# Performance work log

Hardware: AMD Instinct MI355X
Metric: run time of the kernel (lower is better)

The kernel has to match this reference:

```python
import jax, jax.numpy as jnp
import numpy as np

N, B, D, Q = 32, 36, 2048, 1024  # batch, objects, v_dim, q_dim


def setup_inputs() -> dict:
    key = jax.random.key(0)
    ks = jax.random.split(key, 6)
    sc = 0.02  # small init so ReLU chains stay well-scaled
    return {
        "v": jax.random.normal(ks[0], (N, B, D), jnp.float32),
        "q": jax.random.normal(ks[1], (N, Q), jnp.float32),
        "W1": jax.random.normal(ks[2], (D, D), jnp.float32) * sc,
        "b1": jnp.zeros((D,), jnp.float32),
        "W2": jax.random.normal(ks[3], (D, D), jnp.float32) * sc,
        "b2": jnp.zeros((D,), jnp.float32),
        "W3": jax.random.normal(ks[4], (Q, D), jnp.float32) * sc,
        "b3": jnp.zeros((D,), jnp.float32),
    }


def reference(v, q, W1, b1, W2, b2, W3, b3):
    # FCNet = ReLU(Linear(.)) with weight-norm folded, dropout=0 (eval).
    # Original calls linear3 twice (linear4 unused bug), so q_emb == q_emb2.
    qe = jax.nn.relu(q @ W3 + b3)  # (N, D)
    # pairs[n,i,j] = v[n,i]*qe[n] + v[n,j]*qe[n]  -> (N, B, B, D)
    pairs = (v[:, :, None, :] + v[:, None, :, :]) * qe[:, None, None, :]
    h = jax.nn.relu(jnp.einsum('nijd,de->nije', pairs, W1) + b1)  # linear1
    x = jnp.sum(h, axis=2)  # sum over j relations -> (N, B, D)
    return jax.nn.relu(x @ W2 + b2)  # linear2
```

## Files before the change

kernel.cpp:

```cpp
#include <hip/hip_runtime.h>
#include <stdint.h>

#define N_BATCH 32
#define B_OBJ   36
#define D_DIM   2048
#define Q_DIM   1024

typedef __bf16 bf16x8 __attribute__((ext_vector_type(8)));
typedef float  f32x4  __attribute__((ext_vector_type(4)));

__device__ __forceinline__ uint16_t f2bf(float f) {
    uint32_t u = __builtin_bit_cast(uint32_t, f);
    uint32_t r = (u + 0x7FFFu + ((u >> 16) & 1u)) >> 16;
    return (uint16_t)r;
}

__device__ __forceinline__ void gld_lds16(const void* g, void* l) {
    __builtin_amdgcn_global_load_lds(
        (const __attribute__((address_space(1))) uint32_t*)g,
        (__attribute__((address_space(3))) uint32_t*)l, 16, 0, 0);
}

__global__ __launch_bounds__(256) void transpose_all(
    const float* __restrict__ W1, const float* __restrict__ W2,
    const float* __restrict__ W3,
    uint16_t* __restrict__ W1t, uint16_t* __restrict__ W2t,
    uint16_t* __restrict__ W3t) {
    __shared__ float tile[64][65];
    int gy = blockIdx.y;
    const float* W; uint16_t* Wt; int K, k0;
    if (gy < 32)      { W = W1; Wt = W1t; K = 2048; k0 = gy * 64; }
    else if (gy < 64) { W = W2; Wt = W2t; K = 2048; k0 = (gy - 32) * 64; }
    else              { W = W3; Wt = W3t; K = 1024; k0 = (gy - 64) * 64; }
    int n0 = blockIdx.x * 64;
    int t = threadIdx.x;
    {
        int r = t >> 4, c = (t & 15) * 4;
#pragma unroll
        for (int p = 0; p < 4; ++p)
            *(float4*)&tile[r + p * 16][c] =
                *(const float4*)&W[(size_t)(k0 + r + p * 16) * 2048 + n0 + c];
    }
    __syncthreads();
    {
        int n = t >> 2, kb = (t & 3) * 16;
#pragma unroll
        for (int g4 = 0; g4 < 4; ++g4) {
            int k = kb + g4 * 4;
            ushort4 o;
            o.x = f2bf(tile[k][n]);     o.y = f2bf(tile[k + 1][n]);
            o.z = f2bf(tile[k + 2][n]); o.w = f2bf(tile[k + 3][n]);
            *(ushort4*)&Wt[(size_t)(n0 + n) * K + k0 + k] = o;
        }
    }
}

__global__ __launch_bounds__(256) void qk_gemm(
    const float* __restrict__ q,
    const uint16_t* __restrict__ W3t,
    float* __restrict__ qpart) {
    __shared__ __align__(16) uint16_t As[32][32];
    __shared__ __align__(16) uint16_t Bs[128][32];
    int t = threadIdx.x, lane = t & 63, wave = t >> 6;
    int l15 = lane & 15, quad = lane >> 4;
    int n0 = blockIdx.x * 128;
    int kbase = blockIdx.y * 256;
    f32x4 acc[2][2] = {};
    int ar = t >> 3, ac = (t & 7) * 4;
    int br = t >> 2, bk = (t & 3) * 8;

    for (int k0 = 0; k0 < 256; k0 += 32) {
        __syncthreads();
        float4 av = *(const float4*)&q[(size_t)ar * Q_DIM + kbase + k0 + ac];
        ushort4 a4;
        a4.x = f2bf(av.x); a4.y = f2bf(av.y); a4.z = f2bf(av.z); a4.w = f2bf(av.w);
        *(ushort4*)&As[ar][ac] = a4;
        *(uint4*)&Bs[br][bk]      = *(const uint4*)&W3t[(size_t)(n0 + br) * Q_DIM + kbase + k0 + bk];
        *(uint4*)&Bs[br + 64][bk] = *(const uint4*)&W3t[(size_t)(n0 + br + 64) * Q_DIM + kbase + k0 + bk];
        __syncthreads();
        bf16x8 af[2], bfr[2];
        af[0]  = *(const bf16x8*)&As[l15][quad * 8];
        af[1]  = *(const bf16x8*)&As[16 + l15][quad * 8];
        bfr[0] = *(const bf16x8*)&Bs[wave * 32 + l15][quad * 8];
        bfr[1] = *(const bf16x8*)&Bs[wave * 32 + 16 + l15][quad * 8];
#pragma unroll
        for (int i = 0; i < 2; ++i)
#pragma unroll
            for (int j = 0; j < 2; ++j)
                acc[i][j] = __builtin_amdgcn_mfma_f32_16x16x32_bf16(af[i], bfr[j], acc[i][j], 0, 0, 0);
    }
    float* dst = qpart + (size_t)blockIdx.y * 32 * D_DIM;
#pragma unroll
    for (int i = 0; i < 2; ++i)
#pragma unroll
        for (int j = 0; j < 2; ++j) {
            int n = n0 + wave * 32 + j * 16 + l15;
#pragma unroll
            for (int r = 0; r < 4; ++r)
                dst[(size_t)(i * 16 + quad * 4 + r) * D_DIM + n] = acc[i][j][r];
        }
}

__global__ __launch_bounds__(128) void qe_make_u(
    const float* __restrict__ qpart, const float* __restrict__ b3,
    const float* __restrict__ v, uint16_t* __restrict__ u) {
    int nb = blockIdx.y;
    int d4 = blockIdx.x * 128 + threadIdx.x;
    const float4* p = (const float4*)qpart;
    size_t base = (size_t)nb * 512 + d4;
    float4 s0 = p[base], s1 = p[16384 + base], s2 = p[32768 + base], s3 = p[49152 + base];
    float4 b = ((const float4*)b3)[d4];
    float4 qe;
    qe.x = fmaxf(s0.x + s1.x + s2.x + s3.x + b.x, 0.f);
    qe.y = fmaxf(s0.y + s1.y + s2.y + s3.y + b.y, 0.f);
    qe.z = fmaxf(s0.z + s1.z + s2.z + s3.z + b.z, 0.f);
    qe.w = fmaxf(s0.w + s1.w + s2.w + s3.w + b.w, 0.f);
    const float4* v4 = (const float4*)v;
    ushort4* u4 = (ushort4*)u;
    size_t rb = (size_t)nb * B_OBJ * 512 + d4;
#pragma unroll 4
    for (int i = 0; i < B_OBJ; ++i) {
        float4 vv = v4[rb + (size_t)i * 512];
        ushort4 o;
        o.x = f2bf(vv.x * qe.x);
        o.y = f2bf(vv.y * qe.y);
        o.z = f2bf(vv.z * qe.z);
        o.w = f2bf(vv.w * qe.w);
        u4[rb + (size_t)i * 512] = o;
    }
}

__global__ __launch_bounds__(512) void gemm_batch(
    const uint16_t* __restrict__ A,
    const uint16_t* __restrict__ Bt,
    const float* __restrict__ bias,
    void* __restrict__ Cv,
    int mode) {
    extern __shared__ __align__(16) uint16_t smem[];
    float* yt = (float*)smem;

    int t = threadIdx.x, lane = t & 63, wave = t >> 6;
    int l15 = lane & 15, quad = lane >> 4;
    int wr = wave >> 2, wc = wave & 3;
    int nbp = blockIdx.y;
    int n0 = blockIdx.x * 128;
    const uint16_t* Ab = A + (size_t)nbp * 72 * D_DIM;

    const uint16_t* gp[7];
    int loff[7];
    int wslot = (lane & 3) ^ ((lane >> 2) & 3);
#pragma unroll
    for (int c = 0; c < 7; ++c) {
        int r = wave + 8 * c;
        if (r < 24) {
            int g = r >> 2, h = r & 3;
            int arow = g * 16 + (lane >> 2) - (g >= 3 ? 12 : 0);
            gp[c] = Ab + (size_t)arow * D_DIM + h * 32 + wslot * 8;
            loff[c] = h * 3072 + g * 512;
        } else {
            int rb = r - 24, g = rb >> 2, h = rb & 3;
            int brow = g * 16 + (lane >> 2);
            gp[c] = Bt + (size_t)(n0 + brow) * D_DIM + h * 32 + wslot * 8;
            loff[c] = 12288 + h * 4096 + g * 512;
        }
    }

    f32x4 acc[3][2] = {};
    int rslot = quad ^ (l15 & 3);

#define STAGE(kk, bi)                                            \
    {                                                            \
        _Pragma("unroll")                                        \
        for (int c = 0; c < 7; ++c)                              \
            gld_lds16(gp[c] + (kk), smem + (bi) * 28672 + loff[c]); \
    }

    STAGE(0, 0);
    STAGE(128, 1);
    asm volatile("s_waitcnt vmcnt(7)" ::: "memory");
    __builtin_amdgcn_s_barrier();

    for (int k = 0; k < 16; ++k) {
        int cur = k & 1;
        const uint16_t* As = smem + cur * 28672;
        const uint16_t* Bs = As + 12288;
#pragma unroll
        for (int s = 0; s < 4; ++s) {
            bf16x8 af[3], bfr[2];
#pragma unroll
            for (int i = 0; i < 3; ++i)
                af[i] = *(const bf16x8*)(As + s * 3072 + (wr * 48 + i * 16 + l15) * 32 + rslot * 8);
#pragma unroll
            for (int j = 0; j < 2; ++j)
                bfr[j] = *(const bf16x8*)(Bs + s * 4096 + (wc * 32 + j * 16 + l15) * 32 + rslot * 8);
#pragma unroll
            for (int i = 0; i < 3; ++i)
#pragma unroll
                for (int j = 0; j < 2; ++j)
                    acc[i][j] = __builtin_amdgcn_mfma_f32_16x16x32_bf16(af[i], bfr[j], acc[i][j], 0, 0, 0);
        }
        if (k == 15) break;
        __builtin_amdgcn_s_barrier();
        if (k < 14) {
            STAGE((k + 2) * 128, cur);
            asm volatile("s_waitcnt vmcnt(7)" ::: "memory");
        } else {
            asm volatile("s_waitcnt vmcnt(0)" ::: "memory");
        }
        __builtin_amdgcn_s_barrier();
    }
#undef STAGE

    if (mode == 0) {
        uint16_t* X = (uint16_t*)Cv;
        __syncthreads();
#pragma unroll
        for (int i = 0; i < 3; ++i)
#pragma unroll
            for (int j = 0; j < 2; ++j)
#pragma unroll
                for (int r = 0; r < 4; ++r)
                    yt[(wr * 48 + i * 16 + quad * 4 + r) * 132 + wc * 32 + j * 16 + l15] = acc[i][j][r];
        __syncthreads();
        int col = t & 127, sub = t >> 7;
        int b = sub >> 1, half = sub & 1;
        float bv = bias[n0 + col];
        float z[36];
#pragma unroll
        for (int j = 0; j < 36; ++j) z[j] = yt[(b * 48 + j) * 132 + col];
#pragma unroll
        for (int ii = 0; ii < 18; ++ii) {
            int i = half * 18 + ii;
            float zi = z[i] + bv;
            float s = 0.f;
#pragma unroll
            for (int j = 0; j < 36; ++j) s += fmaxf(zi + z[j], 0.f);
            X[(size_t)((nbp * 2 + b) * B_OBJ + i) * D_DIM + n0 + col] = f2bf(s);
        }
    } else {
        float* O = (float*)Cv;
#pragma unroll
        for (int i = 0; i < 3; ++i)
#pragma unroll
            for (int r = 0; r < 4; ++r) {
                int obj = i * 16 + quad * 4 + r;
                if (obj < B_OBJ) {
#pragma unroll
                    for (int j = 0; j < 2; ++j) {
                        int cc = n0 + wc * 32 + j * 16 + l15;
                        O[(size_t)((nbp * 2 + wr) * B_OBJ + obj) * D_DIM + cc] =
                            fmaxf(acc[i][j][r] + bias[cc], 0.f);
                    }
                }
            }
    }
}

extern "C" void kernel_launch(void* const* d_in, const int* in_sizes, int n_in,
                              void* d_out, int out_size, void* d_ws, size_t ws_size,
                              hipStream_t stream) {
    const float* v  = (const float*)d_in[0];
    const float* q  = (const float*)d_in[1];
    const float* W1 = (const float*)d_in[2];
    const float* b1 = (const float*)d_in[3];
    const float* W2 = (const float*)d_in[4];
    const float* b2 = (const float*)d_in[5];
    const float* W3 = (const float*)d_in[6];
    const float* b3 = (const float*)d_in[7];
    float* out = (float*)d_out;

    char* ws = (char*)d_ws;
    uint16_t* W1t   = (uint16_t*)(ws + 0);
    uint16_t* W2t   = (uint16_t*)(ws + 8388608);
    uint16_t* W3t   = (uint16_t*)(ws + 16777216);
    uint16_t* u     = (uint16_t*)(ws + 16777216);
    float*    qpart = (float*)   (ws + 21495808);
    uint16_t* x     = (uint16_t*)(ws + 22806528);

    static bool attr_done = false;
    if (!attr_done) {
        (void)hipFuncSetAttribute((const void*)gemm_batch,
                                  hipFuncAttributeMaxDynamicSharedMemorySize, 114688);
        attr_done = true;
    }

    transpose_all<<<dim3(32, 80), 256, 0, stream>>>(W1, W2, W3, W1t, W2t, W3t);

    qk_gemm<<<dim3(16, 4), 256, 0, stream>>>(q, W3t, qpart);

    qe_make_u<<<dim3(4, N_BATCH), 128, 0, stream>>>(qpart, b3, v, u);

    gemm_batch<<<dim3(16, 16), 512, 114688, stream>>>(u, W1t, b1, x, 0);

    gemm_batch<<<dim3(16, 16), 512, 114688, stream>>>(x, W2t, b2, out, 1);
}
```

Measured before the change: 168.3 us.

## Triple-buffer gemm_batch LDS pipeline and drop redundant A-row duplication

Switches the batched GEMM from double to triple buffering in LDS, issuing the next stage's global-to-LDS loads before the MFMA compute and removing one barrier per iteration. The A tile is restaged as 72 unique rows with a 128-wide XOR-swizzled layout instead of 96 rows with duplicated overlap, cutting the A loads per stage from 24 to 18 wave-rows. Per-wave vmcnt waits are adjusted for the uneven load counts. LDS use rises to 150KB, which keeps occupancy at one block per CU but removes a sync point and some redundant traffic.

```diff
diff --git a/kernel.cpp b/kernel.cpp
--- a/kernel.cpp
+++ b/kernel.cpp
@@ -152,47 +152,60 @@
 #pragma unroll
     for (int c = 0; c < 7; ++c) {
         int r = wave + 8 * c;
-        if (r < 24) {
-            int g = r >> 2, h = r & 3;
-            int arow = g * 16 + (lane >> 2) - (g >= 3 ? 12 : 0);
-            gp[c] = Ab + (size_t)arow * D_DIM + h * 32 + wslot * 8;
-            loff[c] = h * 3072 + g * 512;
+        int rr = (r < 50) ? r : 0;
+        if (rr < 18) {
+            int row = rr * 4 + (lane >> 4);
+            gp[c] = Ab + (size_t)row * D_DIM + ((lane & 15) ^ (row & 7)) * 8;
+            loff[c] = rr * 512;
         } else {
-            int rb = r - 24, g = rb >> 2, h = rb & 3;
+            int rb = rr - 18, h = rb >> 3, g = rb & 7;
             int brow = g * 16 + (lane >> 2);
             gp[c] = Bt + (size_t)(n0 + brow) * D_DIM + h * 32 + wslot * 8;
-            loff[c] = 12288 + h * 4096 + g * 512;
+            loff[c] = 9216 + h * 4096 + g * 512;
         }
     }
 
     f32x4 acc[3][2] = {};
+    int axor  = (4 * wr + l15) & 7;
     int rslot = quad ^ (l15 & 3);
 
 #define STAGE(kk, bi)                                            \
     {                                                            \
         _Pragma("unroll")                                        \
         for (int c = 0; c < 7; ++c)                              \
-            gld_lds16(gp[c] + (kk), smem + (bi) * 28672 + loff[c]); \
+            if (wave + 8 * c < 50)                               \
+                gld_lds16(gp[c] + (kk), smem + (bi) * 25600 + loff[c]); \
+    }
+#define WAIT_L()                                                      \
+    {                                                                 \
+        if (wave < 2) asm volatile("s_waitcnt vmcnt(7)" ::: "memory");\
+        else          asm volatile("s_waitcnt vmcnt(6)" ::: "memory");\
     }
 
     STAGE(0, 0);
     STAGE(128, 1);
-    asm volatile("s_waitcnt vmcnt(7)" ::: "memory");
+    WAIT_L();
     __builtin_amdgcn_s_barrier();
 
+    int cur = 0;
     for (int k = 0; k < 16; ++k) {
-        int cur = k & 1;
-        const uint16_t* As = smem + cur * 28672;
-        const uint16_t* Bs = As + 12288;
+        if (k < 14) {
+            int stb = (cur >= 1) ? cur - 1 : 2;
+            STAGE((k + 2) * 128, stb);
+        }
+        const uint16_t* As = smem + cur * 25600;
+        const uint16_t* Bs = As + 9216;
 #pragma unroll
         for (int s = 0; s < 4; ++s) {
             bf16x8 af[3], bfr[2];
 #pragma unroll
             for (int i = 0; i < 3; ++i)
-                af[i] = *(const bf16x8*)(As + s * 3072 + (wr * 48 + i * 16 + l15) * 32 + rslot * 8);
+                af[i] = *(const bf16x8*)(As + (wr * 36 + i * 16 + l15) * 128 +
+                                         ((4 * s + quad) ^ axor) * 8);
 #pragma unroll
             for (int j = 0; j < 2; ++j)
-                bfr[j] = *(const bf16x8*)(Bs + s * 4096 + (wc * 32 + j * 16 + l15) * 32 + rslot * 8);
+                bfr[j] = *(const bf16x8*)(Bs + s * 4096 +
+                                          (wc * 32 + j * 16 + l15) * 32 + rslot * 8);
 #pragma unroll
             for (int i = 0; i < 3; ++i)
 #pragma unroll
@@ -200,16 +213,16 @@
                     acc[i][j] = __builtin_amdgcn_mfma_f32_16x16x32_bf16(af[i], bfr[j], acc[i][j], 0, 0, 0);
         }
         if (k == 15) break;
-        __builtin_amdgcn_s_barrier();
         if (k < 14) {
-            STAGE((k + 2) * 128, cur);
-            asm volatile("s_waitcnt vmcnt(7)" ::: "memory");
+            WAIT_L();
         } else {
             asm volatile("s_waitcnt vmcnt(0)" ::: "memory");
         }
         __builtin_amdgcn_s_barrier();
+        cur = (cur < 2) ? cur + 1 : 0;
     }
 #undef STAGE
+#undef WAIT_L
 
     if (mode == 0) {
         uint16_t* X = (uint16_t*)Cv;
@@ -280,7 +293,7 @@
     static bool attr_done = false;
     if (!attr_done) {
         (void)hipFuncSetAttribute((const void*)gemm_batch,
-                                  hipFuncAttributeMaxDynamicSharedMemorySize, 114688);
+                                  hipFuncAttributeMaxDynamicSharedMemorySize, 153600);
         attr_done = true;
     }
 
@@ -290,7 +303,7 @@
 
     qe_make_u<<<dim3(4, N_BATCH), 128, 0, stream>>>(qpart, b3, v, u);
 
-    gemm_batch<<<dim3(16, 16), 512, 114688, stream>>>(u, W1t, b1, x, 0);
-
-    gemm_batch<<<dim3(16, 16), 512, 114688, stream>>>(x, W2t, b2, out, 1);
-}
+    gemm_batch<<<dim3(16, 16), 512, 153600, stream>>>(u, W1t, b1, x, 0);
+
+    gemm_batch<<<dim3(16, 16), 512, 153600, stream>>>(x, W2t, b2, out, 1);
+}
```

Measured after the change: 170.1 us. No clear change (+1.1%).

## Load GEMM B operand directly into registers and shrink LDS staging

Applied to the files above, without the earlier changes.

The batched GEMM now loads the weight (B) fragments straight from global memory into registers each k-step instead of staging them through LDS. Only the A tile goes through LDS, double-buffered with a new XOR swizzle, which cuts dynamic shared memory from 112KB to 52KB. The launch bounds now request more resident blocks. The aim is higher occupancy and less LDS traffic. In exchange, B global loads are no longer shared across waves, which raises redundant global/L2 reads and exposes their latency inside each iteration.

```diff
diff --git a/kernel.cpp b/kernel.cpp
--- a/kernel.cpp
+++ b/kernel.cpp
@@ -130,7 +130,7 @@
     }
 }
 
-__global__ __launch_bounds__(512) void gemm_batch(
+__global__ __launch_bounds__(512, 4) void gemm_batch(
     const uint16_t* __restrict__ A,
     const uint16_t* __restrict__ Bt,
     const float* __restrict__ bias,
@@ -146,70 +146,76 @@
     int n0 = blockIdx.x * 128;
     const uint16_t* Ab = A + (size_t)nbp * 72 * D_DIM;
 
-    const uint16_t* gp[7];
-    int loff[7];
-    int wslot = (lane & 3) ^ ((lane >> 2) & 3);
-#pragma unroll
-    for (int c = 0; c < 7; ++c) {
+    const uint16_t* gpa[3];
+    int ra[3];
+#pragma unroll
+    for (int c = 0; c < 3; ++c) {
         int r = wave + 8 * c;
-        if (r < 24) {
-            int g = r >> 2, h = r & 3;
-            int arow = g * 16 + (lane >> 2) - (g >= 3 ? 12 : 0);
-            gp[c] = Ab + (size_t)arow * D_DIM + h * 32 + wslot * 8;
-            loff[c] = h * 3072 + g * 512;
-        } else {
-            int rb = r - 24, g = rb >> 2, h = rb & 3;
-            int brow = g * 16 + (lane >> 2);
-            gp[c] = Bt + (size_t)(n0 + brow) * D_DIM + h * 32 + wslot * 8;
-            loff[c] = 12288 + h * 4096 + g * 512;
-        }
-    }
+        int rr = (r < 18) ? r : 0;
+        int row = rr * 4 + (lane >> 4);
+        gpa[c] = Ab + (size_t)row * D_DIM + ((lane & 15) ^ (row & 7)) * 8;
+        ra[c] = r;
+    }
+    int L = (wave < 2) ? 3 : 2;
+
+    const uint16_t* bp[2];
+#pragma unroll
+    for (int j = 0; j < 2; ++j)
+        bp[j] = Bt + (size_t)(n0 + wc * 32 + j * 16 + l15) * D_DIM + quad * 8;
 
     f32x4 acc[3][2] = {};
-    int rslot = quad ^ (l15 & 3);
-
-#define STAGE(kk, bi)                                            \
-    {                                                            \
-        _Pragma("unroll")                                        \
-        for (int c = 0; c < 7; ++c)                              \
-            gld_lds16(gp[c] + (kk), smem + (bi) * 28672 + loff[c]); \
-    }
-
-    STAGE(0, 0);
-    STAGE(128, 1);
-    asm volatile("s_waitcnt vmcnt(7)" ::: "memory");
-    __builtin_amdgcn_s_barrier();
+    int axor = (4 * wr + l15) & 7;
+
+#define STAGE_A(kk, bi)                                              \
+    {                                                                \
+        _Pragma("unroll")                                            \
+        for (int c = 0; c < 3; ++c)                                  \
+            if (ra[c] < 18)                                          \
+                gld_lds16(gpa[c] + (kk), smem + (bi) * 9216 + ra[c] * 512); \
+    }
+#define WAIT_L()                                                      \
+    {                                                                 \
+        if (wave < 2) asm volatile("s_waitcnt vmcnt(3)" ::: "memory");\
+        else          asm volatile("s_waitcnt vmcnt(2)" ::: "memory");\
+    }
+
+    STAGE_A(0, 0);
 
     for (int k = 0; k < 16; ++k) {
         int cur = k & 1;
-        const uint16_t* As = smem + cur * 28672;
-        const uint16_t* Bs = As + 12288;
-#pragma unroll
-        for (int s = 0; s < 4; ++s) {
-            bf16x8 af[3], bfr[2];
-#pragma unroll
-            for (int i = 0; i < 3; ++i)
-                af[i] = *(const bf16x8*)(As + s * 3072 + (wr * 48 + i * 16 + l15) * 32 + rslot * 8);
-#pragma unroll
-            for (int j = 0; j < 2; ++j)
-                bfr[j] = *(const bf16x8*)(Bs + s * 4096 + (wc * 32 + j * 16 + l15) * 32 + rslot * 8);
-#pragma unroll
-            for (int i = 0; i < 3; ++i)
-#pragma unroll
-                for (int j = 0; j < 2; ++j)
-                    acc[i][j] = __builtin_amdgcn_mfma_f32_16x16x32_bf16(af[i], bfr[j], acc[i][j], 0, 0, 0);
-        }
-        if (k == 15) break;
-        __builtin_amdgcn_s_barrier();
-        if (k < 14) {
-            STAGE((k + 2) * 128, cur);
-            asm volatile("s_waitcnt vmcnt(7)" ::: "memory");
+        int k0 = k * 128;
+        uint4 breg[2][4];
+#pragma unroll
+        for (int j = 0; j < 2; ++j)
+#pragma unroll
+            for (int s = 0; s < 4; ++s)
+                breg[j][s] = *(const uint4*)(bp[j] + k0 + s * 32);
+        if (k < 15) {
+            STAGE_A((k + 1) * 128, cur ^ 1);
+            WAIT_L();
         } else {
             asm volatile("s_waitcnt vmcnt(0)" ::: "memory");
         }
         __builtin_amdgcn_s_barrier();
-    }
-#undef STAGE
+        const uint16_t* Asb = smem + cur * 9216;
+#pragma unroll
+        for (int s = 0; s < 4; ++s) {
+            bf16x8 af[3];
+#pragma unroll
+            for (int i = 0; i < 3; ++i)
+                af[i] = *(const bf16x8*)(Asb + (wr * 36 + i * 16 + l15) * 128 +
+                                         ((4 * s + quad) ^ axor) * 8);
+#pragma unroll
+            for (int i = 0; i < 3; ++i)
+#pragma unroll
+                for (int j = 0; j < 2; ++j)
+                    acc[i][j] = __builtin_amdgcn_mfma_f32_16x16x32_bf16(
+                        af[i], __builtin_bit_cast(bf16x8, breg[j][s]), acc[i][j], 0, 0, 0);
+        }
+        if (k < 15) __builtin_amdgcn_s_barrier();
+    }
+#undef STAGE_A
+#undef WAIT_L
 
     if (mode == 0) {
         uint16_t* X = (uint16_t*)Cv;
@@ -280,7 +286,7 @@
     static bool attr_done = false;
     if (!attr_done) {
         (void)hipFuncSetAttribute((const void*)gemm_batch,
-                                  hipFuncAttributeMaxDynamicSharedMemorySize, 114688);
+                                  hipFuncAttributeMaxDynamicSharedMemorySize, 53248);
         attr_done = true;
     }
 
@@ -290,7 +296,7 @@
 
     qe_make_u<<<dim3(4, N_BATCH), 128, 0, stream>>>(qpart, b3, v, u);
 
-    gemm_batch<<<dim3(16, 16), 512, 114688, stream>>>(u, W1t, b1, x, 0);
-
-    gemm_batch<<<dim3(16, 16), 512, 114688, stream>>>(x, W2t, b2, out, 1);
-}
+    gemm_batch<<<dim3(16, 16), 512, 53248, stream>>>(u, W1t, b1, x, 0);
+
+    gemm_batch<<<dim3(16, 16), 512, 53248, stream>>>(x, W2t, b2, out, 1);
+}
```

Result: slower. 214.6 us (+27.5%).
